# Performance work log

Measured on AMD Instinct MI355X. Metric: run time of the kernel, lower is better.

Reference implementation:

```python
import jax, jax.numpy as jnp
import numpy as np

N, E, IN, H, OUT, L = 50000, 640000, 64, 128, 128, 4
EPS = 1e-8


def setup_inputs() -> dict:
    key = jax.random.key(0)
    ks = jax.random.split(key, 14)
    rn = lambda k, shp: (jax.random.normal(k, shp, jnp.float32) * 0.05)
    return {
        "h": jax.random.normal(ks[0], (N, IN), jnp.float32),
        "pos": jax.random.normal(ks[1], (N, 3), jnp.float32),
        "edge_index": jax.random.randint(ks[2], (2, E), 0, N),
        "emb_W": rn(ks[3], (IN, H)), "emb_b": jnp.zeros((H,), jnp.float32),
        "msg_W1": rn(ks[4], (L, 2 * H + 1, H)), "msg_b1": jnp.zeros((L, H), jnp.float32),
        "msg_W2": rn(ks[5], (L, H, H)), "msg_b2": jnp.zeros((L, H), jnp.float32),
        "coord_W1": rn(ks[6], (L, H, H)), "coord_b1": jnp.zeros((L, H), jnp.float32),
        "coord_W2": rn(ks[7], (L, H, 1)), "coord_b2": jnp.zeros((L, 1), jnp.float32),
        "node_W1": rn(ks[8], (L, 2 * H, H)), "node_b1": jnp.zeros((L, H), jnp.float32),
        "node_W2": rn(ks[9], (L, H, H)), "node_b2": jnp.zeros((L, H), jnp.float32),
        "out_W1": rn(ks[10], (H, H)), "out_b1": jnp.zeros((H,), jnp.float32),
        "out_W2": rn(ks[11], (H, OUT)), "out_b2": jnp.zeros((OUT,), jnp.float32),
    }


def _egnn_forward(h, pos, src, dst, emb_W, emb_b, msg_W1, msg_b1, msg_W2, msg_b2,
                  coord_W1, coord_b1, coord_W2, coord_b2, node_W1, node_b1,
                  node_W2, node_b2, out_W1, out_b1, out_W2, out_b2):
    n = h.shape[0]
    h = h @ emb_W + emb_b  # node embedding [N, H]
    for l in range(L):
        hi, hj = h[dst], h[src]                     # target i, source j gathers [Etot, H]
        rel = pos[src] - pos[dst]                   # row - col (used for coord update)
        dist = jnp.linalg.norm(rel, axis=-1, keepdims=True)  # symmetric, same as |pos_i - pos_j|
        # message MLP: Linear -> SiLU -> Linear -> SiLU on [h_i, h_j, dist]
        m = jax.nn.silu(jnp.concatenate([hi, hj, dist], axis=-1) @ msg_W1[l] + msg_b1[l])
        m = jax.nn.silu(m @ msg_W2[l] + msg_b2[l])
        agg = jax.ops.segment_sum(m, dst, num_segments=n)  # scatter-add to targets
        # coord update: weights from h[row]=h_j, scatter to col=dst
        w = jax.nn.silu(hj @ coord_W1[l] + coord_b1[l]) @ coord_W2[l] + coord_b2[l]  # [Etot,1]
        coord_diff = w * rel / (dist + EPS)
        pos = pos + jax.ops.segment_sum(coord_diff, dst, num_segments=n)
        # node update with residual
        nh = jax.nn.silu(jnp.concatenate([h, agg], axis=-1) @ node_W1[l] + node_b1[l]) @ node_W2[l] + node_b2[l]
        h = h + nh
    out = jax.nn.silu(h @ out_W1 + out_b1) @ out_W2 + out_b2
    return out, pos


def reference(h, pos, edge_index, emb_W, emb_b, msg_W1, msg_b1, msg_W2, msg_b2,
              coord_W1, coord_b1, coord_W2, coord_b2, node_W1, node_b1,
              node_W2, node_b2, out_W1, out_b1, out_W2, out_b2):
    n = h.shape[0]
    loops = jnp.arange(n)  # add_self_loops
    src = jnp.concatenate([edge_index[0], loops])
    dst = jnp.concatenate([edge_index[1], loops])
    return _egnn_forward(h, pos, src, dst, emb_W, emb_b, msg_W1, msg_b1, msg_W2,
                         msg_b2, coord_W1, coord_b1, coord_W2, coord_b2, node_W1,
                         node_b1, node_W2, node_b2, out_W1, out_b1, out_W2, out_b2)
```

## Files before the change

kernel.cpp:

```cpp
#include <hip/hip_runtime.h>
#include <hip/hip_bf16.h>

#define EPSV 1e-8f

typedef short bf16x8 __attribute__((ext_vector_type(8)));
typedef float f32x4  __attribute__((ext_vector_type(4)));

__device__ __forceinline__ float silu_f(float x) {
    return x * __builtin_amdgcn_rcpf(1.0f + __expf(-x));
}
__device__ __forceinline__ float bf2f(short v) {
    return __uint_as_float(((unsigned int)(unsigned short)v) << 16);
}
__device__ __forceinline__ short f2bfs(float f) {
    __hip_bfloat16 h = __float2bfloat16(f);
    return *(short*)&h;
}

#define MAXM 24
struct PackArgs {
    const float* src[MAXM];
    unsigned int doff[MAXM];
    int nchunk[MAXM];
    int nmat;
};

__global__ __launch_bounds__(256) void repack_kernel(PackArgs pa, __hip_bfloat16* base)
{
    int bid = blockIdx.x;
    int m = 0, c = bid;
    while (m < pa.nmat && c >= pa.nchunk[m]) { c -= pa.nchunk[m]; ++m; }
    const float* src = pa.src[m];
    __hip_bfloat16* dst = base + pa.doff[m] + (size_t)c * 4096;
    for (int o = threadIdx.x; o < 4096; o += 256) {
        int j = o & 7, n = (o >> 3) & 127, g = o >> 10;
        dst[o] = __float2bfloat16(src[(size_t)(c * 32 + g * 8 + j) * 128 + n]);
    }
}

__global__ __launch_bounds__(256) void hist_kernel(
    const int* __restrict__ ei, int* __restrict__ cnt, int E, int N)
{
    int e = blockIdx.x * 256 + threadIdx.x;
    int Etot = E + N;
    if (e < Etot) {
        int d = (e < E) ? ei[E + e] : (e - E);
        atomicAdd(&cnt[d], 1);
    }
}

__global__ __launch_bounds__(256) void scan_block_kernel(
    const int* __restrict__ cnt, int* __restrict__ off, int* __restrict__ part, int n)
{
    __shared__ int sdata[256];
    const int tid = threadIdx.x;
    const int base = blockIdx.x * 4096 + tid * 16;
    int loc[16]; int s = 0;
    #pragma unroll
    for (int i = 0; i < 16; ++i) {
        int idx = base + i;
        int v = (idx < n) ? cnt[idx] : 0;
        loc[i] = s; s += v;
    }
    sdata[tid] = s;
    __syncthreads();
    for (int st = 1; st < 256; st <<= 1) {
        int v = (tid >= st) ? sdata[tid - st] : 0;
        __syncthreads();
        sdata[tid] += v;
        __syncthreads();
    }
    int texc = (tid > 0) ? sdata[tid - 1] : 0;
    #pragma unroll
    for (int i = 0; i < 16; ++i) {
        int idx = base + i;
        if (idx < n) off[idx] = texc + loc[i];
    }
    if (tid == 255) part[blockIdx.x] = sdata[255];
}

__global__ void scan_part_kernel(int* part, int np)
{
    if (threadIdx.x == 0 && blockIdx.x == 0) {
        int run = 0;
        for (int i = 0; i < np; ++i) { int v = part[i]; part[i] = run; run += v; }
    }
}

__global__ __launch_bounds__(256) void scan_add_kernel(
    int* __restrict__ off, const int* __restrict__ part, int n)
{
    int idx = blockIdx.x * 4096 + threadIdx.x * 16;
    int p = part[blockIdx.x];
    #pragma unroll
    for (int i = 0; i < 16; ++i)
        if (idx + i < n) off[idx + i] += p;
}

__global__ __launch_bounds__(256) void scatter_kernel(
    const int* __restrict__ ei, int* __restrict__ off,
    int* __restrict__ esrc, int* __restrict__ edst, int E, int N)
{
    int e = blockIdx.x * 256 + threadIdx.x;
    int Etot = E + N;
    if (e < Etot) {
        int s, d;
        if (e < E) { s = ei[e]; d = ei[E + e]; }
        else       { s = d = e - E; }
        int p = atomicAdd(&off[d], 1);
        esrc[p] = s; edst[p] = d;
    }
}

template<int LDA>
__device__ __forceinline__ void mfma_gemm(const __hip_bfloat16 (*At)[LDA], int acol0,
                                          const __hip_bfloat16* __restrict__ Bp,
                                          int kchunks, int w, int lane, f32x4 acc[4][2])
{
    const int ar = lane & 15, g = lane >> 4;
    const int bc = w * 32 + (lane & 15);
    for (int c = 0; c < kchunks; ++c) {
        const int ao = acol0 + c * 32 + g * 8;
        bf16x8 a0 = *(const bf16x8*)&At[ar +  0][ao];
        bf16x8 a1 = *(const bf16x8*)&At[ar + 16][ao];
        bf16x8 a2 = *(const bf16x8*)&At[ar + 32][ao];
        bf16x8 a3 = *(const bf16x8*)&At[ar + 48][ao];
        const __hip_bfloat16* bb = Bp + ((size_t)((c * 4 + g) * 128) + bc) * 8;
        bf16x8 b0 = *(const bf16x8*)(bb);
        bf16x8 b1 = *(const bf16x8*)(bb + 128);
        acc[0][0] = __builtin_amdgcn_mfma_f32_16x16x32_bf16(a0, b0, acc[0][0], 0, 0, 0);
        acc[1][0] = __builtin_amdgcn_mfma_f32_16x16x32_bf16(a1, b0, acc[1][0], 0, 0, 0);
        acc[2][0] = __builtin_amdgcn_mfma_f32_16x16x32_bf16(a2, b0, acc[2][0], 0, 0, 0);
        acc[3][0] = __builtin_amdgcn_mfma_f32_16x16x32_bf16(a3, b0, acc[3][0], 0, 0, 0);
        acc[0][1] = __builtin_amdgcn_mfma_f32_16x16x32_bf16(a0, b1, acc[0][1], 0, 0, 0);
        acc[1][1] = __builtin_amdgcn_mfma_f32_16x16x32_bf16(a1, b1, acc[1][1], 0, 0, 0);
        acc[2][1] = __builtin_amdgcn_mfma_f32_16x16x32_bf16(a2, b1, acc[2][1], 0, 0, 0);
        acc[3][1] = __builtin_amdgcn_mfma_f32_16x16x32_bf16(a3, b1, acc[3][1], 0, 0, 0);
    }
}

__device__ __forceinline__ void zacc(f32x4 acc[4][2]) {
    #pragma unroll
    for (int r = 0; r < 4; ++r)
        #pragma unroll
        for (int c = 0; c < 2; ++c) acc[r][c] = (f32x4){0.f, 0.f, 0.f, 0.f};
}

__device__ __forceinline__ void gemm4x4(const float* __restrict__ Wg,
                                        const float* a0p, const float* a1p,
                                        const float* a2p, const float* a3p,
                                        int K, int o0, float acc[4][4]) {
    for (int k = 0; k < K; k += 4) {
        float4 a0 = *(const float4*)(a0p + k);
        float4 a1 = *(const float4*)(a1p + k);
        float4 a2 = *(const float4*)(a2p + k);
        float4 a3 = *(const float4*)(a3p + k);
        float4 w0 = *(const float4*)(Wg + (k + 0) * 128 + o0);
        float4 w1 = *(const float4*)(Wg + (k + 1) * 128 + o0);
        float4 w2 = *(const float4*)(Wg + (k + 2) * 128 + o0);
        float4 w3 = *(const float4*)(Wg + (k + 3) * 128 + o0);
        float av[4][4] = {{a0.x, a0.y, a0.z, a0.w}, {a1.x, a1.y, a1.z, a1.w},
                          {a2.x, a2.y, a2.z, a2.w}, {a3.x, a3.y, a3.z, a3.w}};
        float wv[4][4] = {{w0.x, w0.y, w0.z, w0.w}, {w1.x, w1.y, w1.z, w1.w},
                          {w2.x, w2.y, w2.z, w2.w}, {w3.x, w3.y, w3.z, w3.w}};
        #pragma unroll
        for (int i = 0; i < 4; ++i)
            #pragma unroll
            for (int kk = 0; kk < 4; ++kk)
                #pragma unroll
                for (int j = 0; j < 4; ++j)
                    acc[i][j] = fmaf(av[i][kk], wv[kk][j], acc[i][j]);
    }
}

__global__ __launch_bounds__(256) void embed_kernel(
    const float* __restrict__ hin, const float* __restrict__ W,
    const float* __restrict__ b, float* __restrict__ hbuf,
    __hip_bfloat16* __restrict__ h16, int N)
{
    __shared__ float in_tile[32][68];
    const int t = threadIdx.x;
    const int nb = blockIdx.x * 32;

    #pragma unroll
    for (int it = 0; it < 2; ++it) {
        int flat = t + 256 * it;
        int c = flat & 15, e = flat >> 4;
        int node = nb + e; if (node >= N) node = N - 1;
        *(float4*)(&in_tile[e][c * 4]) = *(const float4*)(hin + (size_t)node * 64 + c * 4);
    }
    __syncthreads();

    const int o0 = (t & 31) * 4;
    const int e0 = (t >> 5) * 4;
    float acc[4][4];
    #pragma unroll
    for (int i = 0; i < 4; ++i)
        #pragma unroll
        for (int j = 0; j < 4; ++j) acc[i][j] = 0.f;
    gemm4x4(W, &in_tile[e0][0], &in_tile[e0 + 1][0], &in_tile[e0 + 2][0], &in_tile[e0 + 3][0],
            64, o0, acc);
    float4 bv = *(const float4*)(b + o0);
    #pragma unroll
    for (int i = 0; i < 4; ++i) {
        int node = nb + e0 + i;
        if (node < N) {
            float v0 = acc[i][0] + bv.x, v1 = acc[i][1] + bv.y;
            float v2 = acc[i][2] + bv.z, v3 = acc[i][3] + bv.w;
            *(float4*)(&hbuf[(size_t)node * 128 + o0]) = make_float4(v0, v1, v2, v3);
            __hip_bfloat16* hp = h16 + (size_t)node * 128 + o0;
            hp[0] = __float2bfloat16(v0); hp[1] = __float2bfloat16(v1);
            hp[2] = __float2bfloat16(v2); hp[3] = __float2bfloat16(v3);
        }
    }
}

__global__ __launch_bounds__(256) void precompute_kernel(
    const __hip_bfloat16* __restrict__ h16,
    const __hip_bfloat16* __restrict__ W1p,
    const float* __restrict__ b1,
    const __hip_bfloat16* __restrict__ cW1p,
    const float* __restrict__ cb1, const float* __restrict__ cW2,
    const float* __restrict__ cb2,
    __hip_bfloat16* __restrict__ U16, __hip_bfloat16* __restrict__ V16,
    float* __restrict__ wnum, int N)
{
    __shared__ __hip_bfloat16 a8[64][136];
    __shared__ float redw[64][4];
    const int t = threadIdx.x;
    const int nb = blockIdx.x * 64;
    const int lane = t & 63, w = t >> 6, g = lane >> 4, l15 = lane & 15;

    #pragma unroll
    for (int it = 0; it < 4; ++it) {
        int flat = t + 256 * it;
        int c = flat & 15, e = flat >> 4;
        int node = nb + e; if (node >= N) node = N - 1;
        *(int4*)(&a8[e][c * 8]) = *(const int4*)(h16 + (size_t)node * 128 + c * 8);
    }
    __syncthreads();

    const int colA = w * 32 + l15, colB = colA + 16;
    f32x4 acc[4][2];

    zacc(acc);
    mfma_gemm<136>(a8, 0, W1p, 4, w, lane, acc);
    {
        float bA = b1[colA], bB = b1[colB];
        #pragma unroll
        for (int r = 0; r < 4; ++r)
            #pragma unroll
            for (int q = 0; q < 4; ++q) {
                int node = nb + r * 16 + g * 4 + q;
                if (node < N) {
                    U16[(size_t)node * 128 + colA] = __float2bfloat16(acc[r][0][q] + bA);
                    U16[(size_t)node * 128 + colB] = __float2bfloat16(acc[r][1][q] + bB);
                }
            }
    }
    zacc(acc);
    mfma_gemm<136>(a8, 0, W1p + 4 * 4096, 4, w, lane, acc);
    #pragma unroll
    for (int r = 0; r < 4; ++r)
        #pragma unroll
        for (int q = 0; q < 4; ++q) {
            int node = nb + r * 16 + g * 4 + q;
            if (node < N) {
                V16[(size_t)node * 128 + colA] = __float2bfloat16(acc[r][0][q]);
                V16[(size_t)node * 128 + colB] = __float2bfloat16(acc[r][1][q]);
            }
        }
    zacc(acc);
    mfma_gemm<136>(a8, 0, cW1p, 4, w, lane, acc);
    {
        float cb1A = cb1[colA], cb1B = cb1[colB];
        float wA = cW2[colA], wB = cW2[colB];
        #pragma unroll
        for (int r = 0; r < 4; ++r)
            #pragma unroll
            for (int q = 0; q < 4; ++q) {
                float p = silu_f(acc[r][0][q] + cb1A) * wA
                        + silu_f(acc[r][1][q] + cb1B) * wB;
                p += __shfl_xor(p, 1);
                p += __shfl_xor(p, 2);
                p += __shfl_xor(p, 4);
                p += __shfl_xor(p, 8);
                if (l15 == 0) redw[r * 16 + g * 4 + q][w] = p;
            }
    }
    __syncthreads();
    if (t < 64 && nb + t < N)
        wnum[nb + t] = redw[t][0] + redw[t][1] + redw[t][2] + redw[t][3] + cb2[0];
}

__global__ __launch_bounds__(512, 4) void edge_kernel(
    const __hip_bfloat16* __restrict__ U16, const __hip_bfloat16* __restrict__ V16,
    const float* __restrict__ wnum, const float* __restrict__ posb,
    const int* __restrict__ esrc, const int* __restrict__ edst,
    const float* __restrict__ W1tail,
    const __hip_bfloat16* __restrict__ W2p, const float* __restrict__ b2,
    float* __restrict__ agg, float* __restrict__ pdel, int Etot)
{
    __shared__ __hip_bfloat16 m1s[128][136];
    __shared__ int   dstl[128];
    __shared__ float relt[3][128], distl[128], wscl[128];

    const int t = threadIdx.x;
    const int eb = blockIdx.x * 128;
    const int lane = t & 63, w = t >> 6;
    const int g = lane >> 4, l15 = lane & 15;

    bf16x8 uvr[4], vvr[4];
    {
        const int c8 = t & 15;
        #pragma unroll
        for (int j = 0; j < 4; ++j) {
            int row = (t >> 4) + 32 * j;
            int e = eb + row;
            int s = 0, d = 0;
            if (e < Etot) { s = esrc[e]; d = edst[e]; }
            uvr[j] = *(const bf16x8*)(U16 + (size_t)d * 128 + c8 * 8);
            vvr[j] = *(const bf16x8*)(V16 + (size_t)s * 128 + c8 * 8);
        }
    }

    if (t < 128) {
        int e = eb + t;
        int s = 0, d = -1;
        if (e < Etot) { s = esrc[e]; d = edst[e]; }
        dstl[t] = d;
        int dd = (d < 0) ? 0 : d;
        float rx = posb[3 * s + 0] - posb[3 * dd + 0];
        float ry = posb[3 * s + 1] - posb[3 * dd + 1];
        float rz = posb[3 * s + 2] - posb[3 * dd + 2];
        float dist = sqrtf(rx * rx + ry * ry + rz * rz);
        relt[0][t] = rx; relt[1][t] = ry; relt[2][t] = rz;
        distl[t] = dist;
        wscl[t] = wnum[s] * __builtin_amdgcn_rcpf(dist + EPSV);
    }
    __syncthreads();

    {
        const int c8 = t & 15;
        float wt[8];
        *(float4*)&wt[0] = *(const float4*)(W1tail + c8 * 8);
        *(float4*)&wt[4] = *(const float4*)(W1tail + c8 * 8 + 4);
        #pragma unroll
        for (int j = 0; j < 4; ++j) {
            int row = (t >> 4) + 32 * j;
            float dv = distl[row];
            bf16x8 res;
            #pragma unroll
            for (int k = 0; k < 8; ++k) {
                float x = bf2f(uvr[j][k]) + bf2f(vvr[j][k]) + dv * wt[k];
                res[k] = f2bfs(silu_f(x));
            }
            *(bf16x8*)(&m1s[row][c8 * 8]) = res;
        }
    }
    __syncthreads();

    const int col = w * 16 + l15;
    f32x4 acc8[8];
    #pragma unroll
    for (int rt = 0; rt < 8; ++rt) acc8[rt] = (f32x4){0.f, 0.f, 0.f, 0.f};
    for (int c = 0; c < 4; ++c) {
        const int ao = c * 32 + g * 8;
        bf16x8 b0 = *(const bf16x8*)(W2p + ((size_t)((c * 4 + g) * 128) + col) * 8);
        #pragma unroll
        for (int rt = 0; rt < 8; ++rt) {
            bf16x8 a = *(const bf16x8*)&m1s[l15 + 16 * rt][ao];
            acc8[rt] = __builtin_amdgcn_mfma_f32_16x16x32_bf16(a, b0, acc8[rt], 0, 0, 0);
        }
    }
    __syncthreads();

    {
        float b2c = b2[col];
        #pragma unroll
        for (int rt = 0; rt < 8; ++rt)
            #pragma unroll
            for (int q = 0; q < 4; ++q) {
                int row = rt * 16 + g * 4 + q;
                m1s[row][col] = __float2bfloat16(silu_f(acc8[rt][q] + b2c));
            }
    }
    __syncthreads();

    {
        int rcol = t & 127, qtr = t >> 7;
        int r0 = qtr * 32;
        float a = 0.f;
        int cur = dstl[r0];
        #pragma unroll 4
        for (int r = r0; r < r0 + 32; ++r) {
            int d = dstl[r];
            if (d != cur) {
                if (cur >= 0) atomicAdd(&agg[(size_t)cur * 128 + rcol], a);
                a = 0.f; cur = d;
            }
            if (d >= 0) a += bf2f(*(const short*)&m1s[r][rcol]);
        }
        if (cur >= 0) atomicAdd(&agg[(size_t)cur * 128 + rcol], a);
    }

    if (t < 384) {
        int e = t / 3, comp = t % 3;
        if (dstl[e] >= 0)
            atomicAdd(&pdel[(size_t)dstl[e] * 3 + comp], wscl[e] * relt[comp][e]);
    }
}

__global__ __launch_bounds__(256) void node_mfma_kernel(
    float* __restrict__ hbuf, __hip_bfloat16* __restrict__ h16,
    const float* __restrict__ agg,
    float* __restrict__ posb, const float* __restrict__ pdel,
    const __hip_bfloat16* __restrict__ W1p, const float* __restrict__ b1,
    const __hip_bfloat16* __restrict__ W2p, const float* __restrict__ b2,
    const __hip_bfloat16* __restrict__ nxtW1p, const float* __restrict__ nxt_b1,
    const __hip_bfloat16* __restrict__ nxt_cW1p, const float* __restrict__ nxt_cb1,
    const float* __restrict__ nxt_cW2, const float* __restrict__ nxt_cb2,
    __hip_bfloat16* __restrict__ U16, __hip_bfloat16* __restrict__ V16,
    float* __restrict__ wnum,
    int N, int doPre)
{
    __shared__ __hip_bfloat16 a_t[64][264];
    __shared__ __hip_bfloat16 us[64][136];
    __shared__ float redw[64][4];
    const int t = threadIdx.x;
    const int nb = blockIdx.x * 64;
    const int lane = t & 63, w = t >> 6, g = lane >> 4, l15 = lane & 15;

    #pragma unroll
    for (int it = 0; it < 4; ++it) {
        int flat = t + 256 * it;
        int c = flat & 15, e = flat >> 4;
        int node = nb + e; if (node >= N) node = N - 1;
        *(int4*)(&a_t[e][c * 8]) = *(const int4*)(h16 + (size_t)node * 128 + c * 8);
    }
    #pragma unroll
    for (int it = 0; it < 8; ++it) {
        int flat = t + 256 * it;
        int c = flat & 31, e = flat >> 5;
        int node = nb + e; if (node >= N) node = N - 1;
        float4 v = *(const float4*)(agg + (size_t)node * 128 + c * 4);
        __hip_bfloat16* p = &a_t[e][128 + c * 4];
        p[0] = __float2bfloat16(v.x); p[1] = __float2bfloat16(v.y);
        p[2] = __float2bfloat16(v.z); p[3] = __float2bfloat16(v.w);
    }
    __syncthreads();

    const int colA = w * 32 + l15, colB = colA + 16;
    f32x4 acc[4][2];

    zacc(acc);
    mfma_gemm<264>(a_t, 0, W1p, 8, w, lane, acc);
    {
        float b1a = b1[colA], b1b = b1[colB];
        #pragma unroll
        for (int r = 0; r < 4; ++r)
            #pragma unroll
            for (int q = 0; q < 4; ++q) {
                int row = r * 16 + g * 4 + q;
                us[row][colA] = __float2bfloat16(silu_f(acc[r][0][q] + b1a));
                us[row][colB] = __float2bfloat16(silu_f(acc[r][1][q] + b1b));
            }
    }
    __syncthreads();

    zacc(acc);
    mfma_gemm<136>(us, 0, W2p, 4, w, lane, acc);
    {
        float b2a = b2[colA], b2b = b2[colB];
        #pragma unroll
        for (int r = 0; r < 4; ++r)
            #pragma unroll
            for (int q = 0; q < 4; ++q) {
                int row = r * 16 + g * 4 + q;
                int node = nb + row;
                if (node < N) {
                    size_t off = (size_t)node * 128;
                    float va = hbuf[off + colA] + acc[r][0][q] + b2a;
                    float vb = hbuf[off + colB] + acc[r][1][q] + b2b;
                    hbuf[off + colA] = va; hbuf[off + colB] = vb;
                    __hip_bfloat16 ha = __float2bfloat16(va), hb = __float2bfloat16(vb);
                    h16[off + colA] = ha; h16[off + colB] = hb;
                    a_t[row][colA] = ha; a_t[row][colB] = hb;
                } else {
                    a_t[row][colA] = __float2bfloat16(0.f);
                    a_t[row][colB] = __float2bfloat16(0.f);
                }
            }
    }
    if (t < 192) {
        int e = t / 3, comp = t % 3;
        int node = nb + e;
        if (node < N) posb[3 * node + comp] += pdel[3 * node + comp];
    }

    if (!doPre) return;
    __syncthreads();

    zacc(acc);
    mfma_gemm<264>(a_t, 0, nxtW1p, 4, w, lane, acc);
    {
        float bA = nxt_b1[colA], bB = nxt_b1[colB];
        #pragma unroll
        for (int r = 0; r < 4; ++r)
            #pragma unroll
            for (int q = 0; q < 4; ++q) {
                int node = nb + r * 16 + g * 4 + q;
                if (node < N) {
                    U16[(size_t)node * 128 + colA] = __float2bfloat16(acc[r][0][q] + bA);
                    U16[(size_t)node * 128 + colB] = __float2bfloat16(acc[r][1][q] + bB);
                }
            }
    }
    zacc(acc);
    mfma_gemm<264>(a_t, 0, nxtW1p + 4 * 4096, 4, w, lane, acc);
    #pragma unroll
    for (int r = 0; r < 4; ++r)
        #pragma unroll
        for (int q = 0; q < 4; ++q) {
            int node = nb + r * 16 + g * 4 + q;
            if (node < N) {
                V16[(size_t)node * 128 + colA] = __float2bfloat16(acc[r][0][q]);
                V16[(size_t)node * 128 + colB] = __float2bfloat16(acc[r][1][q]);
            }
        }
    zacc(acc);
    mfma_gemm<264>(a_t, 0, nxt_cW1p, 4, w, lane, acc);
    {
        float cb1A = nxt_cb1[colA], cb1B = nxt_cb1[colB];
        float wA = nxt_cW2[colA], wB = nxt_cW2[colB];
        #pragma unroll
        for (int r = 0; r < 4; ++r)
            #pragma unroll
            for (int q = 0; q < 4; ++q) {
                float p = silu_f(acc[r][0][q] + cb1A) * wA
                        + silu_f(acc[r][1][q] + cb1B) * wB;
                p += __shfl_xor(p, 1);
                p += __shfl_xor(p, 2);
                p += __shfl_xor(p, 4);
                p += __shfl_xor(p, 8);
                if (l15 == 0) redw[r * 16 + g * 4 + q][w] = p;
            }
    }
    __syncthreads();
    if (t < 64 && nb + t < N)
        wnum[nb + t] = redw[t][0] + redw[t][1] + redw[t][2] + redw[t][3] + nxt_cb2[0];
}

__global__ __launch_bounds__(256) void out_mfma_kernel(
    const __hip_bfloat16* __restrict__ h16,
    const __hip_bfloat16* __restrict__ W1p, const float* __restrict__ b1,
    const __hip_bfloat16* __restrict__ W2p, const float* __restrict__ b2,
    float* __restrict__ outp, int N)
{
    __shared__ __hip_bfloat16 a8[64][136];
    __shared__ __hip_bfloat16 us[64][136];
    const int t = threadIdx.x;
    const int nb = blockIdx.x * 64;
    const int lane = t & 63, w = t >> 6, g = lane >> 4;

    #pragma unroll
    for (int it = 0; it < 4; ++it) {
        int flat = t + 256 * it;
        int c = flat & 15, e = flat >> 4;
        int node = nb + e; if (node >= N) node = N - 1;
        *(int4*)(&a8[e][c * 8]) = *(const int4*)(h16 + (size_t)node * 128 + c * 8);
    }
    __syncthreads();

    const int colA = w * 32 + (lane & 15), colB = colA + 16;
    f32x4 acc[4][2];

    zacc(acc);
    mfma_gemm<136>(a8, 0, W1p, 4, w, lane, acc);
    {
        float b1a = b1[colA], b1b = b1[colB];
        #pragma unroll
        for (int r = 0; r < 4; ++r)
            #pragma unroll
            for (int q = 0; q < 4; ++q) {
                int row = r * 16 + g * 4 + q;
                us[row][colA] = __float2bfloat16(silu_f(acc[r][0][q] + b1a));
                us[row][colB] = __float2bfloat16(silu_f(acc[r][1][q] + b1b));
            }
    }
    __syncthreads();

    zacc(acc);
    mfma_gemm<136>(us, 0, W2p, 4, w, lane, acc);
    {
        float b2a = b2[colA], b2b = b2[colB];
        #pragma unroll
        for (int r = 0; r < 4; ++r)
            #pragma unroll
            for (int q = 0; q < 4; ++q) {
                int row = r * 16 + g * 4 + q;
                int node = nb + row;
                if (node < N) {
                    outp[(size_t)node * 128 + colA] = acc[r][0][q] + b2a;
                    outp[(size_t)node * 128 + colB] = acc[r][1][q] + b2b;
                }
            }
    }
}

extern "C" void kernel_launch(void* const* d_in, const int* in_sizes, int n_in,
                              void* d_out, int out_size, void* d_ws, size_t ws_size,
                              hipStream_t stream)
{
    const float* hin  = (const float*)d_in[0];
    const float* pos  = (const float*)d_in[1];
    const int*   ei   = (const int*)d_in[2];
    const float* embW = (const float*)d_in[3];
    const float* embb = (const float*)d_in[4];
    const float* mW1  = (const float*)d_in[5];
    const float* mb1  = (const float*)d_in[6];
    const float* mW2  = (const float*)d_in[7];
    const float* mb2  = (const float*)d_in[8];
    const float* cW1  = (const float*)d_in[9];
    const float* cb1  = (const float*)d_in[10];
    const float* cW2  = (const float*)d_in[11];
    const float* cb2  = (const float*)d_in[12];
    const float* nW1  = (const float*)d_in[13];
    const float* nb1  = (const float*)d_in[14];
    const float* nW2  = (const float*)d_in[15];
    const float* nb2  = (const float*)d_in[16];
    const float* oW1  = (const float*)d_in[17];
    const float* ob1  = (const float*)d_in[18];
    const float* oW2  = (const float*)d_in[19];
    const float* ob2  = (const float*)d_in[20];

    const int N = in_sizes[0] / 64;
    const int E = in_sizes[2] / 2;
    const int Etot = E + N;

    float* hbuf = (float*)d_ws;
    float* aggb = hbuf + (size_t)N * 128;
    float* posb = aggb + (size_t)N * 128;
    float* pdel = posb + (size_t)N * 3;
    float* wnum = pdel + (size_t)N * 3;
    __hip_bfloat16* h16 = (__hip_bfloat16*)(wnum + N);
    __hip_bfloat16* U16 = h16 + (size_t)N * 128;
    __hip_bfloat16* V16 = U16 + (size_t)N * 128;
    __hip_bfloat16* packed = V16 + (size_t)N * 128;
    int* cnt  = (int*)(packed + 120 * 4096);
    int* soff = cnt + N;
    int* part = soff + N;
    int* esrc = part + 64;
    int* edst = esrc + Etot;
    float* outp = (float*)d_out;

    PackArgs pa;
    int nm = 0; unsigned int poff = 0; int totalChunks = 0;
    auto addm = [&](const float* s, int kc) {
        pa.src[nm] = s; pa.doff[nm] = poff; pa.nchunk[nm] = kc;
        poff += (unsigned int)kc * 4096; totalChunks += kc; ++nm;
    };
    for (int l = 0; l < 4; ++l) {
        addm(mW1 + (size_t)l * 257 * 128, 8);
        addm(mW2 + (size_t)l * 128 * 128, 4);
        addm(cW1 + (size_t)l * 128 * 128, 4);
        addm(nW1 + (size_t)l * 256 * 128, 8);
        addm(nW2 + (size_t)l * 128 * 128, 4);
    }
    addm(oW1, 4);
    addm(oW2, 4);
    pa.nmat = nm;

    const unsigned int LSTRIDE = 28 * 4096;

    hipMemcpyAsync(posb, pos, (size_t)N * 3 * sizeof(float),
                   hipMemcpyDeviceToDevice, stream);
    repack_kernel<<<totalChunks, 256, 0, stream>>>(pa, packed);

    const int scanBlocks = (N + 4095) / 4096;
    hipMemsetAsync(cnt, 0, (size_t)N * sizeof(int), stream);
    hist_kernel<<<(Etot + 255) / 256, 256, 0, stream>>>(ei, cnt, E, N);
    scan_block_kernel<<<scanBlocks, 256, 0, stream>>>(cnt, soff, part, N);
    scan_part_kernel<<<1, 64, 0, stream>>>(part, scanBlocks);
    scan_add_kernel<<<scanBlocks, 256, 0, stream>>>(soff, part, N);
    scatter_kernel<<<(Etot + 255) / 256, 256, 0, stream>>>(ei, soff, esrc, edst, E, N);

    const int nodeBlocks32 = (N + 31) / 32;
    const int nodeBlocks64 = (N + 63) / 64;
    const int edgeBlocks   = (Etot + 127) / 128;

    embed_kernel<<<nodeBlocks32, 256, 0, stream>>>(hin, embW, embb, hbuf, h16, N);

    precompute_kernel<<<nodeBlocks64, 256, 0, stream>>>(
        h16, packed, mb1, packed + 12 * 4096,
        cb1, cW2, cb2, U16, V16, wnum, N);

    for (int l = 0; l < 4; ++l) {
        hipMemsetAsync(aggb, 0, (size_t)N * 128 * sizeof(float), stream);
        hipMemsetAsync(pdel, 0, (size_t)N * 3 * sizeof(float), stream);
        const __hip_bfloat16* lp = packed + (size_t)l * LSTRIDE;
        edge_kernel<<<edgeBlocks, 512, 0, stream>>>(
            U16, V16, wnum, posb, esrc, edst,
            mW1 + (size_t)l * 257 * 128 + 256 * 128,
            lp + 8 * 4096, mb2 + l * 128,
            aggb, pdel, Etot);
        const int ln = (l < 3) ? (l + 1) : l;
        const __hip_bfloat16* lpn = packed + (size_t)ln * LSTRIDE;
        node_mfma_kernel<<<nodeBlocks64, 256, 0, stream>>>(
            hbuf, h16, aggb, posb, pdel,
            lp + 16 * 4096, nb1 + l * 128,
            lp + 24 * 4096, nb2 + l * 128,
            lpn, mb1 + (size_t)ln * 128,
            lpn + 12 * 4096, cb1 + (size_t)ln * 128,
            cW2 + (size_t)ln * 128, cb2 + ln,
            U16, V16, wnum,
            N, (l < 3) ? 1 : 0);
    }
    out_mfma_kernel<<<nodeBlocks64, 256, 0, stream>>>(
        h16, packed + (size_t)4 * LSTRIDE, ob1,
        packed + (size_t)4 * LSTRIDE + 4 * 4096, ob2, outp, N);

    hipMemcpyAsync(outp + (size_t)N * 128, posb, (size_t)N * 3 * sizeof(float),
                   hipMemcpyDeviceToDevice, stream);
}
```

Before: 1.187 ms.

## Shrink edge kernel tile to 64 edges with 256 threads and shared GEMM helper

```diff
diff --git a/kernel.cpp b/kernel.cpp
--- a/kernel.cpp
+++ b/kernel.cpp
@@ -293,7 +293,7 @@
         wnum[nb + t] = redw[t][0] + redw[t][1] + redw[t][2] + redw[t][3] + cb2[0];
 }
 
-__global__ __launch_bounds__(512, 4) void edge_kernel(
+__global__ __launch_bounds__(256) void edge_kernel(
     const __hip_bfloat16* __restrict__ U16, const __hip_bfloat16* __restrict__ V16,
     const float* __restrict__ wnum, const float* __restrict__ posb,
     const int* __restrict__ esrc, const int* __restrict__ edst,
@@ -301,34 +301,19 @@
     const __hip_bfloat16* __restrict__ W2p, const float* __restrict__ b2,
     float* __restrict__ agg, float* __restrict__ pdel, int Etot)
 {
-    __shared__ __hip_bfloat16 m1s[128][136];
-    __shared__ int   dstl[128];
-    __shared__ float relt[3][128], distl[128], wscl[128];
+    __shared__ __hip_bfloat16 m1s[64][136];
+    __shared__ int   srcl[64], dstl[64];
+    __shared__ float relt[3][64], distl[64], wscl[64];
 
     const int t = threadIdx.x;
-    const int eb = blockIdx.x * 128;
-    const int lane = t & 63, w = t >> 6;
-    const int g = lane >> 4, l15 = lane & 15;
-
-    bf16x8 uvr[4], vvr[4];
-    {
-        const int c8 = t & 15;
-        #pragma unroll
-        for (int j = 0; j < 4; ++j) {
-            int row = (t >> 4) + 32 * j;
-            int e = eb + row;
-            int s = 0, d = 0;
-            if (e < Etot) { s = esrc[e]; d = edst[e]; }
-            uvr[j] = *(const bf16x8*)(U16 + (size_t)d * 128 + c8 * 8);
-            vvr[j] = *(const bf16x8*)(V16 + (size_t)s * 128 + c8 * 8);
-        }
-    }
-
-    if (t < 128) {
+    const int eb = blockIdx.x * 64;
+    const int lane = t & 63, w = t >> 6, g = lane >> 4, l15 = lane & 15;
+
+    if (t < 64) {
         int e = eb + t;
         int s = 0, d = -1;
         if (e < Etot) { s = esrc[e]; d = edst[e]; }
-        dstl[t] = d;
+        srcl[t] = s; dstl[t] = d;
         int dd = (d < 0) ? 0 : d;
         float rx = posb[3 * s + 0] - posb[3 * dd + 0];
         float ry = posb[3 * s + 1] - posb[3 * dd + 1];
@@ -340,71 +325,69 @@
     }
     __syncthreads();
 
-    {
-        const int c8 = t & 15;
-        float wt[8];
-        *(float4*)&wt[0] = *(const float4*)(W1tail + c8 * 8);
-        *(float4*)&wt[4] = *(const float4*)(W1tail + c8 * 8 + 4);
-        #pragma unroll
-        for (int j = 0; j < 4; ++j) {
-            int row = (t >> 4) + 32 * j;
+    #pragma unroll
+    for (int j = 0; j < 4; ++j) {
+        int f = t + 256 * j;
+        int c8 = f & 15, row = f >> 4;
+        bf16x8 res;
+        if (dstl[row] >= 0) {
+            int s = srcl[row], d = dstl[row];
+            bf16x8 uv = *(const bf16x8*)(U16 + (size_t)d * 128 + c8 * 8);
+            bf16x8 vv = *(const bf16x8*)(V16 + (size_t)s * 128 + c8 * 8);
+            float wt[8];
+            *(float4*)&wt[0] = *(const float4*)(W1tail + c8 * 8);
+            *(float4*)&wt[4] = *(const float4*)(W1tail + c8 * 8 + 4);
             float dv = distl[row];
-            bf16x8 res;
             #pragma unroll
             for (int k = 0; k < 8; ++k) {
-                float x = bf2f(uvr[j][k]) + bf2f(vvr[j][k]) + dv * wt[k];
+                float x = bf2f(uv[k]) + bf2f(vv[k]) + dv * wt[k];
                 res[k] = f2bfs(silu_f(x));
             }
-            *(bf16x8*)(&m1s[row][c8 * 8]) = res;
+        } else {
+            #pragma unroll
+            for (int k = 0; k < 8; ++k) res[k] = 0;
         }
-    }
-    __syncthreads();
-
-    const int col = w * 16 + l15;
-    f32x4 acc8[8];
-    #pragma unroll
-    for (int rt = 0; rt < 8; ++rt) acc8[rt] = (f32x4){0.f, 0.f, 0.f, 0.f};
-    for (int c = 0; c < 4; ++c) {
-        const int ao = c * 32 + g * 8;
-        bf16x8 b0 = *(const bf16x8*)(W2p + ((size_t)((c * 4 + g) * 128) + col) * 8);
-        #pragma unroll
-        for (int rt = 0; rt < 8; ++rt) {
-            bf16x8 a = *(const bf16x8*)&m1s[l15 + 16 * rt][ao];
-            acc8[rt] = __builtin_amdgcn_mfma_f32_16x16x32_bf16(a, b0, acc8[rt], 0, 0, 0);
-        }
-    }
-    __syncthreads();
-
-    {
-        float b2c = b2[col];
-        #pragma unroll
-        for (int rt = 0; rt < 8; ++rt)
-            #pragma unroll
-            for (int q = 0; q < 4; ++q) {
-                int row = rt * 16 + g * 4 + q;
-                m1s[row][col] = __float2bfloat16(silu_f(acc8[rt][q] + b2c));
-            }
-    }
-    __syncthreads();
-
-    {
-        int rcol = t & 127, qtr = t >> 7;
-        int r0 = qtr * 32;
+        *(bf16x8*)(&m1s[row][c8 * 8]) = res;
+    }
+    __syncthreads();
+
+    const int colA = w * 32 + l15, colB = colA + 16;
+    f32x4 acc[4][2];
+    zacc(acc);
+    mfma_gemm<136>(m1s, 0, W2p, 4, w, lane, acc);
+    __syncthreads();
+
+    {
+        float b2a = b2[colA], b2b = b2[colB];
+        #pragma unroll
+        for (int r = 0; r < 4; ++r)
+            #pragma unroll
+            for (int q = 0; q < 4; ++q) {
+                int row = r * 16 + g * 4 + q;
+                m1s[row][colA] = __float2bfloat16(silu_f(acc[r][0][q] + b2a));
+                m1s[row][colB] = __float2bfloat16(silu_f(acc[r][1][q] + b2b));
+            }
+    }
+    __syncthreads();
+
+    {
+        int col = t & 127, half = t >> 7;
+        int r0 = half * 32;
         float a = 0.f;
         int cur = dstl[r0];
         #pragma unroll 4
         for (int r = r0; r < r0 + 32; ++r) {
             int d = dstl[r];
             if (d != cur) {
-                if (cur >= 0) atomicAdd(&agg[(size_t)cur * 128 + rcol], a);
+                if (cur >= 0) atomicAdd(&agg[(size_t)cur * 128 + col], a);
                 a = 0.f; cur = d;
             }
-            if (d >= 0) a += bf2f(*(const short*)&m1s[r][rcol]);
+            if (d >= 0) a += bf2f(*(const short*)&m1s[r][col]);
         }
-        if (cur >= 0) atomicAdd(&agg[(size_t)cur * 128 + rcol], a);
-    }
-
-    if (t < 384) {
+        if (cur >= 0) atomicAdd(&agg[(size_t)cur * 128 + col], a);
+    }
+
+    if (t < 192) {
         int e = t / 3, comp = t % 3;
         if (dstl[e] >= 0)
             atomicAdd(&pdel[(size_t)dstl[e] * 3 + comp], wscl[e] * relt[comp][e]);
@@ -687,7 +670,7 @@
 
     const int nodeBlocks32 = (N + 31) / 32;
     const int nodeBlocks64 = (N + 63) / 64;
-    const int edgeBlocks   = (Etot + 127) / 128;
+    const int edgeBlocks   = (Etot + 63) / 64;
 
     embed_kernel<<<nodeBlocks32, 256, 0, stream>>>(hin, embW, embb, hbuf, h16, N);
 
@@ -699,7 +682,7 @@
         hipMemsetAsync(aggb, 0, (size_t)N * 128 * sizeof(float), stream);
         hipMemsetAsync(pdel, 0, (size_t)N * 3 * sizeof(float), stream);
         const __hip_bfloat16* lp = packed + (size_t)l * LSTRIDE;
-        edge_kernel<<<edgeBlocks, 512, 0, stream>>>(
+        edge_kernel<<<edgeBlocks, 256, 0, stream>>>(
             U16, V16, wnum, posb, esrc, edst,
             mW1 + (size_t)l * 257 * 128 + 256 * 128,
             lp + 8 * 4096, mb2 + l * 128,
```

Result: faster. 1.032 ms (-13.0%).
